# Performance work log

Measured on AMD Instinct MI355X. Metric: run time of the kernel, lower is better.

## Reference

```python
import jax, jax.numpy as jnp
from jax import lax
import numpy as np

ATTN = 32  # attn_size window
PAD, SOS = 1, 2


def setup_inputs() -> dict:
    key = jax.random.key(0)
    ks = jax.random.split(key, 20)
    B, L, V, E, H = 16, 64, 32000, 512, 512
    sc = 0.02
    inp = {
        "s_tensor": jax.random.randint(ks[0], (B, L), 0, V, dtype=jnp.int32),
        "parents_tensor": jax.random.randint(ks[1], (L,), 0, L, dtype=jnp.int32),
        "emb": jax.random.normal(ks[2], (V, E), jnp.float32) * sc,
        "W_hid": jax.random.normal(ks[3], (H, H), jnp.float32) * sc,
        "b_hid": jnp.zeros((H,), jnp.float32),
        "v_w": jax.random.normal(ks[4], (H,), jnp.float32) * sc,
        "v_b": jnp.zeros((1,), jnp.float32),
        "W_ctx": jax.random.normal(ks[5], (E + H, H), jnp.float32) * sc,
        "b_ctx": jnp.zeros((H,), jnp.float32),
        "W_ih": jax.random.normal(ks[6], (H, 4 * H), jnp.float32) * sc,
        "W_hh": jax.random.normal(ks[7], (H, 4 * H), jnp.float32) * sc,
        "b_lstm": jnp.zeros((4 * H,), jnp.float32),
        "W_glob": jax.random.normal(ks[8], (3 * H, V), jnp.float32) * sc,
        "b_glob": jnp.zeros((V,), jnp.float32),
        "w_sw": jax.random.normal(ks[9], (2 * H,), jnp.float32) * sc,
        "b_sw": jnp.zeros((1,), jnp.float32),
    }
    return inp


def _decode(emb, W_hid, b_hid, v_w, v_b, W_ctx, b_ctx, W_ih, W_hh, b_lstm,
            W_glob, b_glob, w_sw, b_sw, s_tensor, parents_tensor):
    B, L = s_tensor.shape
    H = W_hid.shape[0]
    A = ATTN
    # teacher forcing: input at step t is SOS for t=0, else s_tensor[:, t-1]
    inputs = jnp.concatenate(
        [jnp.full((B, 1), SOS, s_tensor.dtype), s_tensor[:, : L - 2]], axis=1)  # [B, L-1]
    targets = s_tensor[:, 1:]  # [B, L-1]
    hs_buf0 = jnp.zeros((B, A + L, H), jnp.float32)  # past decoder hidden states (A zero-pad prefix)
    h0 = jnp.zeros((B, H), jnp.float32)
    c0 = jnp.zeros((B, H), jnp.float32)

    def step(carry, xs):
        h, c, hs_buf = carry
        tok, tgt, par, t = xs
        x = emb[tok]  # [B, E]
        # memory = last A decoder hidden states (steps t-A .. t-1)
        mem = lax.dynamic_slice(hs_buf, (0, t, 0), (B, A, H))
        # Bahdanau-style scores: v^T tanh(W_hidden(h) + mem), masked to valid window
        q = h @ W_hid + b_hid  # [B, H]
        scores = jnp.tanh(q[:, None, :] + mem) @ v_w + v_b  # [B, A]
        valid = jnp.arange(A) >= (A - t)
        scores = jnp.where(valid[None, :], scores, -1e20)
        attn = jax.nn.softmax(scores, axis=1)
        context = jnp.einsum('ba,bah->bh', attn, mem)
        hid = jax.nn.selu(jnp.concatenate([x, context], axis=1) @ W_ctx + b_ctx)
        # single-step LSTM cell (PyTorch gate order i,f,g,o)
        gates = hid @ W_ih + h @ W_hh + b_lstm
        i, f, g, o = jnp.split(gates, 4, axis=1)
        c_new = jax.nn.sigmoid(f) * c + jax.nn.sigmoid(i) * jnp.tanh(g)
        h_new = jax.nn.sigmoid(o) * jnp.tanh(c_new)
        # parent hidden state
        p = jnp.clip(par, 0, jnp.maximum(t - 1, 0))
        h_par = lax.dynamic_slice(hs_buf, (0, A + p, 0), (B, 1, H))[:, 0]
        logits = jnp.concatenate([h_new, c_new, h_par], axis=1) @ W_glob + b_glob
        logp = jax.nn.log_softmax(logits, axis=1)
        s = jax.nn.sigmoid(jnp.concatenate([h_new, c_new], axis=1) @ w_sw + b_sw)  # [B,1]
        out = s[:, None] * logp if s.ndim == 1 else s * logp  # pointer switch on global dist
        nll = -jnp.take_along_axis(out, tgt[:, None].astype(jnp.int32), axis=1)[:, 0]
        nll = jnp.where(tgt != PAD, nll, 0.0)
        pred = jnp.argmax(out, axis=1).astype(jnp.int32)
        hs_buf = lax.dynamic_update_slice(hs_buf, h_new[:, None, :], (0, A + t, 0))
        return (h_new, c_new, hs_buf), (nll, pred)

    T = L - 1
    xs = (inputs.T, targets.T, parents_tensor[:T], jnp.arange(T, dtype=jnp.int32))
    _, (nlls, preds) = lax.scan(step, (h0, c0, hs_buf0), xs)
    loss = nlls.sum() / B
    return loss, preds.T  # [B, L-1] predicted tokens


def reference(s_tensor, parents_tensor, emb, W_hid, b_hid, v_w, v_b, W_ctx, b_ctx,
              W_ih, W_hh, b_lstm, W_glob, b_glob, w_sw, b_sw):
    return _decode(emb, W_hid, b_hid, v_w, v_b, W_ctx, b_ctx, W_ih, W_hh, b_lstm,
                   W_glob, b_glob, w_sw, b_sw, s_tensor, parents_tensor)
```

## Files before the change

kernel.cpp:

```cpp
#include <hip/hip_runtime.h>
#include <math.h>

#define BB 16
#define LL 64
#define TT 63
#define HH 512
#define AA 32
#define VV 32000
#define NCHUNK 250
#define CHW 128
#define TGRP 3
#define NTG 21
#define PAD_TOK 1
#define SOS_TOK 2
#define HSROW 96
#define ZK 1536
#define FLTMAX 3.402823466e38f

__device__ __forceinline__ float sigm(float x){ return 1.0f/(1.0f + __expf(-x)); }

__global__ __launch_bounds__(256) void k_pre(const int* __restrict__ s, const float* __restrict__ emb,
                      const float* __restrict__ Wctx, const float* __restrict__ bctx,
                      float* __restrict__ xwpre)
{
    int t = blockIdx.x >> 3;
    int jc = blockIdx.x & 7;
    int tid = threadIdx.x;
    int jj = tid & 63, bq = tid >> 6;
    int j = jc*64 + jj;
    __shared__ int toks[BB];
    __shared__ float xs[BB][HH];
    if (tid < BB) {
        int b = tid;
        toks[b] = (t == 0) ? SOS_TOK : s[b*LL + (t-1)];
    }
    __syncthreads();
    for (int i = tid; i < BB*HH; i += 256) {
        int b = i >> 9, k = i & 511;
        xs[b][k] = emb[(size_t)toks[b]*HH + k];
    }
    __syncthreads();
    float acc[4];
    #pragma unroll
    for (int u = 0; u < 4; u++) acc[u] = bctx[j];
    for (int k = 0; k < HH; k += 4) {
        float w0 = Wctx[(k+0)*HH+j], w1 = Wctx[(k+1)*HH+j],
              w2 = Wctx[(k+2)*HH+j], w3 = Wctx[(k+3)*HH+j];
        #pragma unroll
        for (int u = 0; u < 4; u++) {
            int b = bq*4 + u;
            float4 hv = *reinterpret_cast<const float4*>(&xs[b][k]);
            acc[u] = fmaf(hv.x, w0, acc[u]);
            acc[u] = fmaf(hv.y, w1, acc[u]);
            acc[u] = fmaf(hv.z, w2, acc[u]);
            acc[u] = fmaf(hv.w, w3, acc[u]);
        }
    }
    #pragma unroll
    for (int u = 0; u < 4; u++) {
        int b = bq*4 + u;
        xwpre[((size_t)t*BB + b)*HH + j] = acc[u];
    }
}

__global__ __launch_bounds__(256) void k_tw(const float* __restrict__ Wg, float4* __restrict__ Wt4b)
{
    int kg = blockIdx.x / 125;
    int cb = blockIdx.x % 125;
    int col = cb*256 + threadIdx.x;
    const float* w0 = Wg + (size_t)(4*kg)*VV + col;
    float4 v;
    v.x = w0[0];
    v.y = w0[VV];
    v.z = w0[2*VV];
    v.w = w0[3*VV];
    Wt4b[(size_t)(col >> 6)*(384*64) + kg*64 + (col & 63)] = v;
}

__global__ __launch_bounds__(256) void k_twl(const float* __restrict__ W, float4* __restrict__ WT)
{
    int kg = blockIdx.x >> 3;
    int cb = blockIdx.x & 7;
    int col = cb*256 + threadIdx.x;
    const float* w0 = W + (size_t)(4*kg)*2048 + col;
    float4 v;
    v.x = w0[0];
    v.y = w0[2048];
    v.z = w0[2*2048];
    v.w = w0[3*2048];
    WT[(size_t)kg*2048 + col] = v;
}

__device__ void finish_step(int tp, int b, int tid,
                            const int* __restrict__ s,
                            const float* __restrict__ lb,
                            const float* __restrict__ pmax,
                            const float* __restrict__ spart,
                            const float* __restrict__ bsw,
                            float* __restrict__ nll, float* __restrict__ out,
                            float* cv, int* ci, double* sdd, float* extra)
{
    float v = -FLTMAX;
    if (tid < NCHUNK) v = pmax[tid*BB + b];
    cv[tid] = v; __syncthreads();
    for (int sft = 256; sft >= 1; sft >>= 1) {
        if (tid < sft) cv[tid] = fmaxf(cv[tid], cv[tid+sft]);
        __syncthreads();
    }
    float gmax = cv[0];
    __syncthreads();

    const float* Lb = lb + (size_t)b*VV;
    double sd = 0.0;
    for (int col = tid; col < VV; col += 512) {
        float d1 = Lb[col] - gmax;
        double u = (double)d1, e;
        if (u < -0.25) {
            e = exp(u);
        } else {
            e = 1.0 + u*(1.0/7.0);
            e = 1.0 + u*e*(1.0/6.0);
            e = 1.0 + u*e*(1.0/5.0);
            e = 1.0 + u*e*(1.0/4.0);
            e = 1.0 + u*e*(1.0/3.0);
            e = 1.0 + u*e*(1.0/2.0);
            e = 1.0 + u*e;
        }
        sd += e;
    }
    sdd[tid] = sd; __syncthreads();
    for (int sft = 256; sft >= 1; sft >>= 1) {
        if (tid < sft) sdd[tid] += sdd[tid+sft];
        __syncthreads();
    }
    float logS = logf((float)sdd[0]);

    float z = bsw[0];
    #pragma unroll
    for (int i2 = 0; i2 < 8; i2++) z += spart[b*8 + i2];
    float sF = 1.0f/(1.0f + expf(-z));
    __syncthreads();

    int tg = s[b*LL + tp + 1];
    float best = -FLTMAX; int bidx = 0x7fffffff;
    for (int col = tid; col < VV; col += 512) {
        float d1 = Lb[col] - gmax;
        float d2 = d1 - logS;
        float pq = sF * d2;
        if (pq > best) { best = pq; bidx = col; }
        if (col == tg) extra[0] = pq;
    }
    cv[tid] = best; ci[tid] = bidx; __syncthreads();
    for (int sft = 256; sft >= 1; sft >>= 1) {
        if (tid < sft) {
            float v2 = cv[tid+sft]; int i2 = ci[tid+sft];
            if (v2 > cv[tid] || (v2 == cv[tid] && i2 < ci[tid])) { cv[tid] = v2; ci[tid] = i2; }
        }
        __syncthreads();
    }
    if (tid == 0) {
        out[1 + b*TT + tp] = (float)ci[0];
        nll[tp*BB + b] = (tg != PAD_TOK) ? -extra[0] : 0.f;
    }
    __syncthreads();
}

__global__ __launch_bounds__(512) void k_fin_all(
    int t0, const int* __restrict__ s,
    const float* __restrict__ lbBase, unsigned long long lbStride,
    const float* __restrict__ pmaxBase, unsigned long long pmaxStride,
    const float* __restrict__ spartAll, const float* __restrict__ bsw,
    float* __restrict__ nll, float* __restrict__ out)
{
    __shared__ float cv[512];
    __shared__ int   ci[512];
    __shared__ double sdd[512];
    __shared__ float extra[2];
    int idx = blockIdx.x >> 4;
    int tp = t0 + idx, b = blockIdx.x & 15;
    finish_step(tp, b, threadIdx.x, s,
                lbBase + (size_t)idx * lbStride,
                pmaxBase + (size_t)idx * pmaxStride,
                spartAll + (size_t)tp * 128,
                bsw, nll, out, cv, ci, sdd, extra);
}

__global__ __launch_bounds__(512) void k_attn(
    int t,
    const float* __restrict__ Whid, const float* __restrict__ bhid,
    const float* __restrict__ vw, const float* __restrict__ vb,
    const float* __restrict__ Wctx, const float* __restrict__ xwpre,
    const float* __restrict__ hs, float* __restrict__ hidg)
{
    int b = blockIdx.x, tid = threadIdx.x;
    __shared__ float hsh[HH], qs[HH], ctxs[HH];
    __shared__ float sc[AA], at[AA];
    const float* hp = hs + ((size_t)b*HSROW + (AA + t - 1))*HH;
    hsh[tid] = hp[tid];
    __syncthreads();
    {
        int j = tid;
        float acc = bhid[j];
        for (int k = 0; k < HH; k += 4) {
            float4 hv = *reinterpret_cast<const float4*>(&hsh[k]);
            acc = fmaf(hv.x, Whid[(k+0)*HH+j], acc);
            acc = fmaf(hv.y, Whid[(k+1)*HH+j], acc);
            acc = fmaf(hv.z, Whid[(k+2)*HH+j], acc);
            acc = fmaf(hv.w, Whid[(k+3)*HH+j], acc);
        }
        qs[j] = acc;
    }
    __syncthreads();
    {
        int w = tid >> 6, lane = tid & 63;
        for (int r = 0; r < 4; r++) {
            int a = w + 8*r;
            const float* mem = hs + ((size_t)b*HSROW + (t + a))*HH;
            float p = 0.f;
            for (int j = lane; j < HH; j += 64) p += tanhf(qs[j] + mem[j]) * vw[j];
            for (int m = 32; m >= 1; m >>= 1) p += __shfl_xor(p, m);
            if (lane == 0) sc[a] = (a >= AA - t) ? (p + vb[0]) : -1e20f;
        }
    }
    __syncthreads();
    if (tid < 64) {
        float v = (tid < 32) ? sc[tid] : -FLTMAX;
        float m = v;
        for (int sh = 16; sh >= 1; sh >>= 1) m = fmaxf(m, __shfl_xor(m, sh));
        float e = (tid < 32) ? __expf(v - m) : 0.f;
        float ss = e;
        for (int sh = 16; sh >= 1; sh >>= 1) ss += __shfl_xor(ss, sh);
        if (tid < 32) at[tid] = e / ss;
    }
    __syncthreads();
    {
        int j = tid;
        float ctx = 0.f;
        for (int a = 0; a < AA; a++)
            ctx += at[a] * hs[((size_t)b*HSROW + (t + a))*HH + j];
        ctxs[j] = ctx;
    }
    __syncthreads();
    {
        int j = tid;
        float acc = xwpre[((size_t)t*BB + b)*HH + j];
        const float* W2 = Wctx + (size_t)HH*HH;
        for (int k = 0; k < HH; k += 4) {
            float4 hv = *reinterpret_cast<const float4*>(&ctxs[k]);
            acc = fmaf(hv.x, W2[(k+0)*HH+j], acc);
            acc = fmaf(hv.y, W2[(k+1)*HH+j], acc);
            acc = fmaf(hv.z, W2[(k+2)*HH+j], acc);
            acc = fmaf(hv.w, W2[(k+3)*HH+j], acc);
        }
        const float scl = 1.0507009873554805f, al = 1.6732632423543772f;
        hidg[b*HH + j] = (acc > 0.f) ? scl*acc : scl*al*expm1f(acc);
    }
}

__global__ __launch_bounds__(256) void k_gates(
    int t, const int* __restrict__ parents,
    const float4* __restrict__ WihT, const float4* __restrict__ WhhT,
    const float* __restrict__ blstm, const float* __restrict__ wsw,
    const float* __restrict__ hidg, float* __restrict__ hs,
    float* __restrict__ cvec, float* __restrict__ spart,
    float* __restrict__ zbuf)
{
    int bid = blockIdx.x, b = bid >> 3, hc = bid & 7, h0 = hc*64;
    int tid = threadIdx.x, g = tid >> 6, jj = tid & 63, j = h0 + jj, col = g*HH + j;
    __shared__ float hid_s[HH], h_s[HH];
    __shared__ float gsl[4][64];
    const float* hp = hs + ((size_t)b*HSROW + (AA + t - 1))*HH;
    for (int k = tid; k < HH; k += 256) { hid_s[k] = hidg[b*HH + k]; h_s[k] = hp[k]; }
    __syncthreads();
    float acc = blstm[col];
    #pragma unroll 8
    for (int kg = 0; kg < 128; kg++) {
        float4 w = WihT[(size_t)kg*2048 + col];
        float4 hv = *reinterpret_cast<const float4*>(&hid_s[kg*4]);
        acc = fmaf(hv.x, w.x, acc);
        acc = fmaf(hv.y, w.y, acc);
        acc = fmaf(hv.z, w.z, acc);
        acc = fmaf(hv.w, w.w, acc);
    }
    #pragma unroll 8
    for (int kg = 0; kg < 128; kg++) {
        float4 w = WhhT[(size_t)kg*2048 + col];
        float4 hv = *reinterpret_cast<const float4*>(&h_s[kg*4]);
        acc = fmaf(hv.x, w.x, acc);
        acc = fmaf(hv.y, w.y, acc);
        acc = fmaf(hv.z, w.z, acc);
        acc = fmaf(hv.w, w.w, acc);
    }
    gsl[g][jj] = acc;
    __syncthreads();
    if (tid >= 64 && tid < 128) {
        int jj2 = tid - 64;
        int par = parents[t];
        int tm1 = (t - 1 > 0) ? (t - 1) : 0;
        int p = (par < 0) ? 0 : ((par > tm1) ? tm1 : par);
        float v = (t == 0) ? 0.f : hs[((size_t)b*HSROW + (AA + p))*HH + h0 + jj2];
        zbuf[(size_t)b*ZK + 2*HH + h0 + jj2] = v;
    }
    if (tid < 64) {
        float gi = gsl[0][jj], gf = gsl[1][jj], gg = gsl[2][jj], go = gsl[3][jj];
        float cp = cvec[b*HH + j];
        float cn = sigm(gf)*cp + sigm(gi)*tanhf(gg);
        float hn = sigm(go)*tanhf(cn);
        cvec[b*HH + j] = cn;
        hs[((size_t)b*HSROW + (AA + t))*HH + j] = hn;
        zbuf[(size_t)b*ZK + j] = hn;
        zbuf[(size_t)b*ZK + HH + j] = cn;
        float sp = hn*wsw[j] + cn*wsw[HH + j];
        for (int m = 32; m >= 1; m >>= 1) sp += __shfl_xor(sp, m);
        if (jj == 0) spart[b*8 + hc] = sp;
    }
}

template<int NT>
__device__ __forceinline__ void logits_body6(int chunk, int base_t,
    const float4* __restrict__ Wt4b, const float* __restrict__ bg,
    const float* __restrict__ zBase, size_t zStride,
    float* __restrict__ lbBase, size_t lbStride,
    float* __restrict__ pmaxBase, size_t pmaxStride,
    float* zs)
{
    int tid = threadIdx.x;
    int lane = tid & 63;
    int cg = lane & 31;
    int kh = lane >> 5;
    int b0 = (tid >> 6) * 4;
    const int BUF = NT*16*2*64;

    const float4* wt0 = Wt4b + (size_t)(chunk*2 + 0)*(384*64) + cg;
    const float4* wt1 = Wt4b + (size_t)(chunk*2 + 0)*(384*64) + cg + 32;
    const float4* wt2 = Wt4b + (size_t)(chunk*2 + 1)*(384*64) + cg;
    const float4* wt3 = Wt4b + (size_t)(chunk*2 + 1)*(384*64) + cg + 32;

    float acc[NT][4][4];
    #pragma unroll
    for (int tt = 0; tt < NT; tt++)
        #pragma unroll
        for (int cc = 0; cc < 4; cc++) {
            float binit = (kh == 0) ? bg[chunk*CHW + cg + 32*cc] : 0.f;
            #pragma unroll
            for (int u = 0; u < 4; u++) acc[tt][cc][u] = binit;
        }

    const int NF4 = NT*16*2*16;
    auto STAGE = [&](int sc, float* dst) {
        int kc = sc >> 2, sub = sc & 3;
        #pragma unroll
        for (int p = 0; p < NF4/256; p++) {
            int fi = tid + p*256;
            int kl4 = fi & 15, khs = (fi >> 4) & 1, uu = (fi >> 5) & 15, tt = fi >> 9;
            const float* src = zBase + (size_t)(base_t + tt)*zStride + kc*512
                             + (size_t)uu*ZK + khs*256 + sub*64 + kl4*4;
            *reinterpret_cast<float4*>(&dst[(((tt*16 + uu)*2 + khs)*64) + kl4*4]) =
                *reinterpret_cast<const float4*>(src);
        }
    };

    STAGE(0, zs);
    __syncthreads();
    for (int sc = 0; sc < 12; sc++) {
        float* cur = zs + (sc & 1)*BUF;
        if (sc + 1 < 12) STAGE(sc + 1, zs + ((sc + 1) & 1)*BUF);
        int kc = sc >> 2, sub = sc & 3;
        int kgb = kc*128 + kh*64 + sub*16;
        const float4* w0P = wt0 + (size_t)kgb*64;
        const float4* w1P = wt1 + (size_t)kgb*64;
        const float4* w2P = wt2 + (size_t)kgb*64;
        const float4* w3P = wt3 + (size_t)kgb*64;
        #pragma unroll 4
        for (int kl = 0; kl < 16; kl++) {
            float4 w0 = w0P[kl*64];
            float4 w1 = w1P[kl*64];
            float4 w2 = w2P[kl*64];
            float4 w3 = w3P[kl*64];
            #pragma unroll
            for (int tt = 0; tt < NT; tt++) {
                #pragma unroll
                for (int u = 0; u < 4; u++) {
                    float4 z = *reinterpret_cast<const float4*>(
                        &cur[(((tt*16 + (b0 + u))*2 + kh)*64) + kl*4]);
                    acc[tt][0][u] = fmaf(z.x, w0.x, fmaf(z.y, w0.y, fmaf(z.z, w0.z, fmaf(z.w, w0.w, acc[tt][0][u]))));
                    acc[tt][1][u] = fmaf(z.x, w1.x, fmaf(z.y, w1.y, fmaf(z.z, w1.z, fmaf(z.w, w1.w, acc[tt][1][u]))));
                    acc[tt][2][u] = fmaf(z.x, w2.x, fmaf(z.y, w2.y, fmaf(z.z, w2.z, fmaf(z.w, w2.w, acc[tt][2][u]))));
                    acc[tt][3][u] = fmaf(z.x, w3.x, fmaf(z.y, w3.y, fmaf(z.z, w3.z, fmaf(z.w, w3.w, acc[tt][3][u]))));
                }
            }
        }
        __syncthreads();
    }

    #pragma unroll
    for (int tt = 0; tt < NT; tt++) {
        float* lb   = lbBase   + (size_t)(base_t + tt)*lbStride;
        float* pmax = pmaxBase + (size_t)(base_t + tt)*pmaxStride;
        #pragma unroll
        for (int u = 0; u < 4; u++) {
            float vmax = -FLTMAX;
            #pragma unroll
            for (int cc = 0; cc < 4; cc++) {
                float a = acc[tt][cc][u];
                float oth = __shfl_xor(a, 32);
                float tot = a + oth;
                if (kh == 0) lb[(size_t)(b0 + u)*VV + chunk*CHW + cg + 32*cc] = tot;
                vmax = fmaxf(vmax, tot);
            }
            for (int m = 16; m >= 1; m >>= 1) vmax = fmaxf(vmax, __shfl_xor(vmax, m));
            if (lane == 0) pmax[chunk*BB + b0 + u] = vmax;
        }
    }
}

__global__ __launch_bounds__(256) void k_logits_mega3(
    const float4* __restrict__ Wt4b, const float* __restrict__ bg,
    const float* __restrict__ zBase,
    float* __restrict__ lbBase, float* __restrict__ pmaxBase)
{
    __shared__ float zs[2*TGRP*16*2*64];
    logits_body6<TGRP>(blockIdx.y, blockIdx.x * TGRP, Wt4b, bg,
                       zBase, (size_t)BB*ZK, lbBase, 512000, pmaxBase, 4000, zs);
}

__global__ __launch_bounds__(256) void k_logits_T1(
    const float4* __restrict__ Wt4b, const float* __restrict__ bg,
    const float* __restrict__ zbuf,
    float* __restrict__ lb, float* __restrict__ pmax)
{
    __shared__ float zs[2*1*16*2*64];
    logits_body6<1>(blockIdx.x, 0, Wt4b, bg, zbuf, 0, lb, 0, pmax, 0, zs);
}

__global__ __launch_bounds__(256) void k_logits_F(
    const float* __restrict__ Wg, const float* __restrict__ bg,
    const float* __restrict__ zbuf,
    float* __restrict__ lb, float* __restrict__ pmax)
{
    int tid = threadIdx.x;
    int chunk = blockIdx.x;
    int lane = tid & 63;
    int cg = lane & 31;
    int kh = lane >> 5;
    int b0 = (tid >> 6) * 4;

    float acc[4][4];
    #pragma unroll
    for (int cc = 0; cc < 4; cc++) {
        float binit = (kh == 0) ? bg[chunk*CHW + cg + 32*cc] : 0.f;
        #pragma unroll
        for (int u = 0; u < 4; u++) acc[cc][u] = binit;
    }

    for (int kc = 0; kc < 3; kc++) {
        const float* zb = zbuf + kc*512 + (size_t)b0*ZK;
        #pragma unroll 2
        for (int k4 = 0; k4 < 64; k4++) {
            int kb = kh*256 + k4*4;
            const float* wr = Wg + (size_t)(kc*512 + kb)*VV + chunk*CHW + cg;
            float4 w[4];
            #pragma unroll
            for (int cc = 0; cc < 4; cc++) {
                w[cc].x = wr[32*cc];
                w[cc].y = wr[(size_t)VV + 32*cc];
                w[cc].z = wr[(size_t)2*VV + 32*cc];
                w[cc].w = wr[(size_t)3*VV + 32*cc];
            }
            #pragma unroll
            for (int u = 0; u < 4; u++) {
                float4 z = *reinterpret_cast<const float4*>(&zb[(size_t)u*ZK + kb]);
                #pragma unroll
                for (int cc = 0; cc < 4; cc++)
                    acc[cc][u] = fmaf(z.x, w[cc].x, fmaf(z.y, w[cc].y, fmaf(z.z, w[cc].z, fmaf(z.w, w[cc].w, acc[cc][u]))));
            }
        }
    }

    #pragma unroll
    for (int u = 0; u < 4; u++) {
        float vmax = -FLTMAX;
        #pragma unroll
        for (int cc = 0; cc < 4; cc++) {
            float a = acc[cc][u];
            float oth = __shfl_xor(a, 32);
            float tot = a + oth;
            if (kh == 0) lb[(size_t)(b0 + u)*VV + chunk*CHW + cg + 32*cc] = tot;
            vmax = fmaxf(vmax, tot);
        }
        for (int m = 16; m >= 1; m >>= 1) vmax = fmaxf(vmax, __shfl_xor(vmax, m));
        if (lane == 0) pmax[chunk*BB + b0 + u] = vmax;
    }
}

__global__ __launch_bounds__(256) void k_final_loss(
    const float* __restrict__ nll, float* __restrict__ out)
{
    __shared__ double cs2[256];
    int tid = threadIdx.x;
    double psm = 0.0;
    for (int i = tid; i < TT*BB; i += 256) psm += (double)nll[i];
    cs2[tid] = psm; __syncthreads();
    for (int sft = 128; sft >= 1; sft >>= 1) {
        if (tid < sft) cs2[tid] += cs2[tid+sft];
        __syncthreads();
    }
    if (tid == 0) out[0] = (float)(cs2[0] / (double)BB);
}

extern "C" void kernel_launch(void* const* d_in, const int* in_sizes, int n_in,
                              void* d_out, int out_size, void* d_ws, size_t ws_size,
                              hipStream_t stream)
{
    const int*   s_tok = (const int*)  d_in[0];
    const int*   par   = (const int*)  d_in[1];
    const float* emb   = (const float*)d_in[2];
    const float* Whid  = (const float*)d_in[3];
    const float* bhid  = (const float*)d_in[4];
    const float* vw    = (const float*)d_in[5];
    const float* vb    = (const float*)d_in[6];
    const float* Wctx  = (const float*)d_in[7];
    const float* bctx  = (const float*)d_in[8];
    const float* Wih   = (const float*)d_in[9];
    const float* Whh   = (const float*)d_in[10];
    const float* blstm = (const float*)d_in[11];
    const float* Wg    = (const float*)d_in[12];
    const float* bg    = (const float*)d_in[13];
    const float* wsw   = (const float*)d_in[14];
    const float* bsw   = (const float*)d_in[15];
    float* out = (float*)d_out;

    size_t ws_f = ws_size / sizeof(float);
    const size_t base_f = 786432 + 8192 + 516096 + 8192;
    const size_t com_f  = 8064 + 1008 + 2*1048576;
    const size_t full_f = base_f + com_f + (size_t)63*4000 + (size_t)63*512000
                        + (size_t)63*24576 + 49152000;
    const size_t mid_f  = base_f + com_f + 4000 + 512000 + 24576 + 49152000;
    int mode = (ws_f >= full_f) ? 2 : ((ws_f >= mid_f) ? 1 : 0);

    float* ws = (float*)d_ws;
    size_t off = 0;
    float* hs      = ws + off; off += 786432;
    float* cvec    = ws + off; off += 8192;
    float* xwpre   = ws + off; off += 516096;
    float* hidg    = ws + off; off += 8192;
    float* pmaxAll = ws + off; off += (mode == 2) ? (size_t)63*4000 : 4000;
    float* spartAll= ws + off; off += 8064;
    float* nll     = ws + off; off += 1008;
    float* zbufAll = ws + off; off += (mode == 2) ? (size_t)63*24576 : 24576;
    float* lbAll   = ws + off; off += (mode == 2) ? (size_t)63*512000 : 512000;
    float4* WihT   = (float4*)(ws + off); off += 1048576;
    float4* WhhT   = (float4*)(ws + off); off += 1048576;
    float4* Wt4b   = (float4*)(ws + off);

    hipMemsetAsync(hs, 0, (786432 + 8192) * sizeof(float), stream);

    hipLaunchKernelGGL(k_twl, dim3(1024), dim3(256), 0, stream, Wih, WihT);
    hipLaunchKernelGGL(k_twl, dim3(1024), dim3(256), 0, stream, Whh, WhhT);
    if (mode >= 1) {
        hipLaunchKernelGGL(k_tw, dim3(384*125), dim3(256), 0, stream, Wg, Wt4b);
    }
    hipLaunchKernelGGL(k_pre, dim3(TT*8), dim3(256), 0, stream, s_tok, emb, Wctx, bctx, xwpre);

    if (mode == 2) {
        for (int t = 0; t < TT; t++) {
            hipLaunchKernelGGL(k_attn, dim3(BB), dim3(512), 0, stream,
                t, Whid, bhid, vw, vb, Wctx, xwpre, hs, hidg);
            hipLaunchKernelGGL(k_gates, dim3(128), dim3(256), 0, stream,
                t, par, WihT, WhhT, blstm, wsw, hidg, hs, cvec,
                spartAll + (size_t)t*128, zbufAll + (size_t)t*BB*ZK);
        }
        hipLaunchKernelGGL(k_logits_mega3, dim3(NTG, NCHUNK), dim3(256), 0, stream,
            Wt4b, bg, zbufAll, lbAll, pmaxAll);
        hipLaunchKernelGGL(k_fin_all, dim3(TT*BB), dim3(512), 0, stream,
            0, s_tok, lbAll, (unsigned long long)512000,
            pmaxAll, (unsigned long long)4000,
            spartAll, bsw, nll, out);
    } else {
        for (int t = 0; t < TT; t++) {
            hipLaunchKernelGGL(k_attn, dim3(BB), dim3(512), 0, stream,
                t, Whid, bhid, vw, vb, Wctx, xwpre, hs, hidg);
            hipLaunchKernelGGL(k_gates, dim3(128), dim3(256), 0, stream,
                t, par, WihT, WhhT, blstm, wsw, hidg, hs, cvec,
                spartAll + (size_t)t*128, zbufAll);
            if (mode >= 1) {
                hipLaunchKernelGGL(k_logits_T1, dim3(NCHUNK), dim3(256), 0, stream,
                    Wt4b, bg, zbufAll, lbAll, pmaxAll);
            } else {
                hipLaunchKernelGGL(k_logits_F, dim3(NCHUNK), dim3(256), 0, stream,
                    Wg, bg, zbufAll, lbAll, pmaxAll);
            }
            hipLaunchKernelGGL(k_fin_all, dim3(BB), dim3(512), 0, stream,
                t, s_tok, lbAll, (unsigned long long)0, pmaxAll, (unsigned long long)0,
                spartAll, bsw, nll, out);
        }
    }
    hipLaunchKernelGGL(k_final_loss, dim3(1), dim3(256), 0, stream, nll, out);
}
```

Before: 4.767 ms.

## Fuse recurrent attention and LSTM steps into one cooperative persistent kernel

Replaces the 126 per-step launches of the attention and gate kernels with one cooperative kernel of 128 blocks that loops over timesteps and uses grid-wide syncs between the attention and gate phases. The attention work is rewritten for 256-thread blocks so it runs inside the persistent grid, on the first 16 blocks. The goal is to remove kernel launch overhead and inter-kernel gaps on the serial recurrence. The trade-off is that attention uses half as many threads per batch row, and each step now pays for two grid barriers. If cooperative launch is unavailable or fails, the old per-step launch loop is used.

After: 13.27 ms. +178.3%, slower.

```diff
diff --git a/kernel.cpp b/kernel.cpp
--- a/kernel.cpp
+++ b/kernel.cpp
@@ -1,5 +1,8 @@
 #include <hip/hip_runtime.h>
+#include <hip/hip_cooperative_groups.h>
 #include <math.h>
+
+namespace cg = cooperative_groups;
 
 #define BB 16
 #define LL 64
@@ -185,21 +188,21 @@
                 bsw, nll, out, cv, ci, sdd, extra);
 }
 
-__global__ __launch_bounds__(512) void k_attn(
-    int t,
+__device__ __forceinline__ void attn256(int t, int ab, int tid,
     const float* __restrict__ Whid, const float* __restrict__ bhid,
     const float* __restrict__ vw, const float* __restrict__ vb,
-    const float* __restrict__ Wctx, const float* __restrict__ xwpre,
-    const float* __restrict__ hs, float* __restrict__ hidg)
-{
-    int b = blockIdx.x, tid = threadIdx.x;
-    __shared__ float hsh[HH], qs[HH], ctxs[HH];
-    __shared__ float sc[AA], at[AA];
-    const float* hp = hs + ((size_t)b*HSROW + (AA + t - 1))*HH;
+    const float* __restrict__ W2, const float* __restrict__ xwpre,
+    const float* __restrict__ hs, float* __restrict__ hidg,
+    float* hsh, float* qs, float* ctxs, float* sc, float* at)
+{
+    const float* hp = hs + ((size_t)ab*HSROW + (AA + t - 1))*HH;
     hsh[tid] = hp[tid];
-    __syncthreads();
-    {
-        int j = tid;
+    hsh[tid + 256] = hp[tid + 256];
+    __syncthreads();
+
+    #pragma unroll
+    for (int jo = 0; jo < HH; jo += 256) {
+        int j = tid + jo;
         float acc = bhid[j];
         for (int k = 0; k < HH; k += 4) {
             float4 hv = *reinterpret_cast<const float4*>(&hsh[k]);
@@ -211,11 +214,12 @@
         qs[j] = acc;
     }
     __syncthreads();
+
     {
         int w = tid >> 6, lane = tid & 63;
-        for (int r = 0; r < 4; r++) {
-            int a = w + 8*r;
-            const float* mem = hs + ((size_t)b*HSROW + (t + a))*HH;
+        for (int r = 0; r < 8; r++) {
+            int a = w + 4*r;
+            const float* mem = hs + ((size_t)ab*HSROW + (t + a))*HH;
             float p = 0.f;
             for (int j = lane; j < HH; j += 64) p += tanhf(qs[j] + mem[j]) * vw[j];
             for (int m = 32; m >= 1; m >>= 1) p += __shfl_xor(p, m);
@@ -223,6 +227,7 @@
         }
     }
     __syncthreads();
+
     if (tid < 64) {
         float v = (tid < 32) ? sc[tid] : -FLTMAX;
         float m = v;
@@ -233,18 +238,21 @@
         if (tid < 32) at[tid] = e / ss;
     }
     __syncthreads();
-    {
-        int j = tid;
+
+    #pragma unroll
+    for (int jo = 0; jo < HH; jo += 256) {
+        int j = tid + jo;
         float ctx = 0.f;
         for (int a = 0; a < AA; a++)
-            ctx += at[a] * hs[((size_t)b*HSROW + (t + a))*HH + j];
+            ctx += at[a] * hs[((size_t)ab*HSROW + (t + a))*HH + j];
         ctxs[j] = ctx;
     }
     __syncthreads();
-    {
-        int j = tid;
-        float acc = xwpre[((size_t)t*BB + b)*HH + j];
-        const float* W2 = Wctx + (size_t)HH*HH;
+
+    #pragma unroll
+    for (int jo = 0; jo < HH; jo += 256) {
+        int j = tid + jo;
+        float acc = xwpre[((size_t)t*BB + ab)*HH + j];
         for (int k = 0; k < HH; k += 4) {
             float4 hv = *reinterpret_cast<const float4*>(&ctxs[k]);
             acc = fmaf(hv.x, W2[(k+0)*HH+j], acc);
@@ -253,25 +261,20 @@
             acc = fmaf(hv.w, W2[(k+3)*HH+j], acc);
         }
         const float scl = 1.0507009873554805f, al = 1.6732632423543772f;
-        hidg[b*HH + j] = (acc > 0.f) ? scl*acc : scl*al*expm1f(acc);
-    }
-}
-
-__global__ __launch_bounds__(256) void k_gates(
-    int t, const int* __restrict__ parents,
+        hidg[ab*HH + j] = (acc > 0.f) ? scl*acc : scl*al*expm1f(acc);
+    }
+}
+
+__device__ __forceinline__ void gates256(int t, int b, int hc, int tid,
+    const int* __restrict__ parents,
     const float4* __restrict__ WihT, const float4* __restrict__ WhhT,
     const float* __restrict__ blstm, const float* __restrict__ wsw,
-    const float* __restrict__ hidg, float* __restrict__ hs,
-    float* __restrict__ cvec, float* __restrict__ spart,
-    float* __restrict__ zbuf)
-{
-    int bid = blockIdx.x, b = bid >> 3, hc = bid & 7, h0 = hc*64;
-    int tid = threadIdx.x, g = tid >> 6, jj = tid & 63, j = h0 + jj, col = g*HH + j;
-    __shared__ float hid_s[HH], h_s[HH];
-    __shared__ float gsl[4][64];
-    const float* hp = hs + ((size_t)b*HSROW + (AA + t - 1))*HH;
-    for (int k = tid; k < HH; k += 256) { hid_s[k] = hidg[b*HH + k]; h_s[k] = hp[k]; }
-    __syncthreads();
+    float* __restrict__ hs, float* __restrict__ cvec,
+    float* __restrict__ spart, float* __restrict__ zbuf,
+    float* hid_s, float* h_s, float (*gsl)[64])
+{
+    int h0 = hc*64;
+    int g = tid >> 6, jj = tid & 63, j = h0 + jj, col = g*HH + j;
     float acc = blstm[col];
     #pragma unroll 8
     for (int kg = 0; kg < 128; kg++) {
@@ -316,6 +319,133 @@
     }
 }
 
+__global__ __launch_bounds__(256) void k_persist(
+    const int* __restrict__ parents,
+    const float* __restrict__ Whid, const float* __restrict__ bhid,
+    const float* __restrict__ vw, const float* __restrict__ vb,
+    const float* __restrict__ Wctx, const float* __restrict__ xwpre,
+    const float4* __restrict__ WihT, const float4* __restrict__ WhhT,
+    const float* __restrict__ blstm, const float* __restrict__ wsw,
+    float* __restrict__ hs, float* __restrict__ cvec,
+    float* __restrict__ spartAll, float* __restrict__ zbufAll,
+    float* __restrict__ hidg)
+{
+    cg::grid_group grid = cg::this_grid();
+    int bid = blockIdx.x, tid = threadIdx.x;
+    int b = bid >> 3, hc = bid & 7;
+    __shared__ float hsh[HH], qs[HH], ctxs[HH], hid_s[HH];
+    __shared__ float sc[AA], at[AA];
+    __shared__ float gsl[4][64];
+    const float* W2 = Wctx + (size_t)HH*HH;
+
+    for (int t = 0; t < TT; t++) {
+        if (bid < BB) {
+            attn256(t, bid, tid, Whid, bhid, vw, vb, W2, xwpre, hs, hidg,
+                    hsh, qs, ctxs, sc, at);
+        }
+        grid.sync();
+
+        const float* hp = hs + ((size_t)b*HSROW + (AA + t - 1))*HH;
+        for (int k = tid; k < HH; k += 256) { hid_s[k] = hidg[b*HH + k]; hsh[k] = hp[k]; }
+        __syncthreads();
+        gates256(t, b, hc, tid, parents, WihT, WhhT, blstm, wsw,
+                 hs, cvec, spartAll + (size_t)t*128, zbufAll + (size_t)t*BB*ZK,
+                 hid_s, hsh, gsl);
+        grid.sync();
+    }
+}
+
+__global__ __launch_bounds__(512) void k_attn(
+    int t,
+    const float* __restrict__ Whid, const float* __restrict__ bhid,
+    const float* __restrict__ vw, const float* __restrict__ vb,
+    const float* __restrict__ Wctx, const float* __restrict__ xwpre,
+    const float* __restrict__ hs, float* __restrict__ hidg)
+{
+    int b = blockIdx.x, tid = threadIdx.x;
+    __shared__ float hsh[HH], qs[HH], ctxs[HH];
+    __shared__ float sc[AA], at[AA];
+    const float* hp = hs + ((size_t)b*HSROW + (AA + t - 1))*HH;
+    hsh[tid] = hp[tid];
+    __syncthreads();
+    {
+        int j = tid;
+        float acc = bhid[j];
+        for (int k = 0; k < HH; k += 4) {
+            float4 hv = *reinterpret_cast<const float4*>(&hsh[k]);
+            acc = fmaf(hv.x, Whid[(k+0)*HH+j], acc);
+            acc = fmaf(hv.y, Whid[(k+1)*HH+j], acc);
+            acc = fmaf(hv.z, Whid[(k+2)*HH+j], acc);
+            acc = fmaf(hv.w, Whid[(k+3)*HH+j], acc);
+        }
+        qs[j] = acc;
+    }
+    __syncthreads();
+    {
+        int w = tid >> 6, lane = tid & 63;
+        for (int r = 0; r < 4; r++) {
+            int a = w + 8*r;
+            const float* mem = hs + ((size_t)b*HSROW + (t + a))*HH;
+            float p = 0.f;
+            for (int j = lane; j < HH; j += 64) p += tanhf(qs[j] + mem[j]) * vw[j];
+            for (int m = 32; m >= 1; m >>= 1) p += __shfl_xor(p, m);
+            if (lane == 0) sc[a] = (a >= AA - t) ? (p + vb[0]) : -1e20f;
+        }
+    }
+    __syncthreads();
+    if (tid < 64) {
+        float v = (tid < 32) ? sc[tid] : -FLTMAX;
+        float m = v;
+        for (int sh = 16; sh >= 1; sh >>= 1) m = fmaxf(m, __shfl_xor(m, sh));
+        float e = (tid < 32) ? __expf(v - m) : 0.f;
+        float ss = e;
+        for (int sh = 16; sh >= 1; sh >>= 1) ss += __shfl_xor(ss, sh);
+        if (tid < 32) at[tid] = e / ss;
+    }
+    __syncthreads();
+    {
+        int j = tid;
+        float ctx = 0.f;
+        for (int a = 0; a < AA; a++)
+            ctx += at[a] * hs[((size_t)b*HSROW + (t + a))*HH + j];
+        ctxs[j] = ctx;
+    }
+    __syncthreads();
+    {
+        int j = tid;
+        float acc = xwpre[((size_t)t*BB + b)*HH + j];
+        const float* W2 = Wctx + (size_t)HH*HH;
+        for (int k = 0; k < HH; k += 4) {
+            float4 hv = *reinterpret_cast<const float4*>(&ctxs[k]);
+            acc = fmaf(hv.x, W2[(k+0)*HH+j], acc);
+            acc = fmaf(hv.y, W2[(k+1)*HH+j], acc);
+            acc = fmaf(hv.z, W2[(k+2)*HH+j], acc);
+            acc = fmaf(hv.w, W2[(k+3)*HH+j], acc);
+        }
+        const float scl = 1.0507009873554805f, al = 1.6732632423543772f;
+        hidg[b*HH + j] = (acc > 0.f) ? scl*acc : scl*al*expm1f(acc);
+    }
+}
+
+__global__ __launch_bounds__(256) void k_gates(
+    int t, const int* __restrict__ parents,
+    const float4* __restrict__ WihT, const float4* __restrict__ WhhT,
+    const float* __restrict__ blstm, const float* __restrict__ wsw,
+    const float* __restrict__ hidg, float* __restrict__ hs,
+    float* __restrict__ cvec, float* __restrict__ spart,
+    float* __restrict__ zbuf)
+{
+    int bid = blockIdx.x, b = bid >> 3, hc = bid & 7;
+    int tid = threadIdx.x;
+    __shared__ float hid_s[HH], h_s[HH];
+    __shared__ float gsl[4][64];
+    const float* hp = hs + ((size_t)b*HSROW + (AA + t - 1))*HH;
+    for (int k = tid; k < HH; k += 256) { hid_s[k] = hidg[b*HH + k]; h_s[k] = hp[k]; }
+    __syncthreads();
+    gates256(t, b, hc, tid, parents, WihT, WhhT, blstm, wsw,
+             hs, cvec, spart, zbuf, hid_s, h_s, gsl);
+}
+
 template<int NT>
 __device__ __forceinline__ void logits_body6(int chunk, int base_t,
     const float4* __restrict__ Wt4b, const float* __restrict__ bg,
@@ -326,29 +456,29 @@
 {
     int tid = threadIdx.x;
     int lane = tid & 63;
-    int cg = lane & 31;
+    int cg2 = lane & 31;
     int kh = lane >> 5;
     int b0 = (tid >> 6) * 4;
     const int BUF = NT*16*2*64;
 
-    const float4* wt0 = Wt4b + (size_t)(chunk*2 + 0)*(384*64) + cg;
-    const float4* wt1 = Wt4b + (size_t)(chunk*2 + 0)*(384*64) + cg + 32;
-    const float4* wt2 = Wt4b + (size_t)(chunk*2 + 1)*(384*64) + cg;
-    const float4* wt3 = Wt4b + (size_t)(chunk*2 + 1)*(384*64) + cg + 32;
+    const float4* wt0 = Wt4b + (size_t)(chunk*2 + 0)*(384*64) + cg2;
+    const float4* wt1 = Wt4b + (size_t)(chunk*2 + 0)*(384*64) + cg2 + 32;
+    const float4* wt2 = Wt4b + (size_t)(chunk*2 + 1)*(384*64) + cg2;
+    const float4* wt3 = Wt4b + (size_t)(chunk*2 + 1)*(384*64) + cg2 + 32;
 
     float acc[NT][4][4];
     #pragma unroll
     for (int tt = 0; tt < NT; tt++)
         #pragma unroll
         for (int cc = 0; cc < 4; cc++) {
-            float binit = (kh == 0) ? bg[chunk*CHW + cg + 32*cc] : 0.f;
+            float binit = (kh == 0) ? bg[chunk*CHW + cg2 + 32*cc] : 0.f;
             #pragma unroll
             for (int u = 0; u < 4; u++) acc[tt][cc][u] = binit;
         }
 
     const int NF4 = NT*16*2*16;
-    auto STAGE = [&](int sc, float* dst) {
-        int kc = sc >> 2, sub = sc & 3;
+    auto STAGE = [&](int sc2, float* dst) {
+        int kc = sc2 >> 2, sub = sc2 & 3;
         #pragma unroll
         for (int p = 0; p < NF4/256; p++) {
             int fi = tid + p*256;
@@ -362,10 +492,10 @@
 
     STAGE(0, zs);
     __syncthreads();
-    for (int sc = 0; sc < 12; sc++) {
-        float* cur = zs + (sc & 1)*BUF;
-        if (sc + 1 < 12) STAGE(sc + 1, zs + ((sc + 1) & 1)*BUF);
-        int kc = sc >> 2, sub = sc & 3;
+    for (int sc2 = 0; sc2 < 12; sc2++) {
+        float* cur = zs + (sc2 & 1)*BUF;
+        if (sc2 + 1 < 12) STAGE(sc2 + 1, zs + ((sc2 + 1) & 1)*BUF);
+        int kc = sc2 >> 2, sub = sc2 & 3;
         int kgb = kc*128 + kh*64 + sub*16;
         const float4* w0P = wt0 + (size_t)kgb*64;
         const float4* w1P = wt1 + (size_t)kgb*64;
@@ -405,7 +535,7 @@
                 float a = acc[tt][cc][u];
                 float oth = __shfl_xor(a, 32);
                 float tot = a + oth;
-                if (kh == 0) lb[(size_t)(b0 + u)*VV + chunk*CHW + cg + 32*cc] = tot;
+                if (kh == 0) lb[(size_t)(b0 + u)*VV + chunk*CHW + cg2 + 32*cc] = tot;
                 vmax = fmaxf(vmax, tot);
             }
             for (int m = 16; m >= 1; m >>= 1) vmax = fmaxf(vmax, __shfl_xor(vmax, m));
@@ -441,14 +571,14 @@
     int tid = threadIdx.x;
     int chunk = blockIdx.x;
     int lane = tid & 63;
-    int cg = lane & 31;
+    int cg2 = lane & 31;
     int kh = lane >> 5;
     int b0 = (tid >> 6) * 4;
 
     float acc[4][4];
     #pragma unroll
     for (int cc = 0; cc < 4; cc++) {
-        float binit = (kh == 0) ? bg[chunk*CHW + cg + 32*cc] : 0.f;
+        float binit = (kh == 0) ? bg[chunk*CHW + cg2 + 32*cc] : 0.f;
         #pragma unroll
         for (int u = 0; u < 4; u++) acc[cc][u] = binit;
     }
@@ -458,7 +588,7 @@
         #pragma unroll 2
         for (int k4 = 0; k4 < 64; k4++) {
             int kb = kh*256 + k4*4;
-            const float* wr = Wg + (size_t)(kc*512 + kb)*VV + chunk*CHW + cg;
+            const float* wr = Wg + (size_t)(kc*512 + kb)*VV + chunk*CHW + cg2;
             float4 w[4];
             #pragma unroll
             for (int cc = 0; cc < 4; cc++) {
@@ -485,7 +615,7 @@
             float a = acc[cc][u];
             float oth = __shfl_xor(a, 32);
             float tot = a + oth;
-            if (kh == 0) lb[(size_t)(b0 + u)*VV + chunk*CHW + cg + 32*cc] = tot;
+            if (kh == 0) lb[(size_t)(b0 + u)*VV + chunk*CHW + cg2 + 32*cc] = tot;
             vmax = fmaxf(vmax, tot);
         }
         for (int m = 16; m >= 1; m >>= 1) vmax = fmaxf(vmax, __shfl_xor(vmax, m));
@@ -563,12 +693,26 @@
     hipLaunchKernelGGL(k_pre, dim3(TT*8), dim3(256), 0, stream, s_tok, emb, Wctx, bctx, xwpre);
 
     if (mode == 2) {
-        for (int t = 0; t < TT; t++) {
-            hipLaunchKernelGGL(k_attn, dim3(BB), dim3(512), 0, stream,
-                t, Whid, bhid, vw, vb, Wctx, xwpre, hs, hidg);
-            hipLaunchKernelGGL(k_gates, dim3(128), dim3(256), 0, stream,
-                t, par, WihT, WhhT, blstm, wsw, hidg, hs, cvec,
-                spartAll + (size_t)t*128, zbufAll + (size_t)t*BB*ZK);
+        int coop = 0;
+        hipDeviceGetAttribute(&coop, hipDeviceAttributeCooperativeLaunch, 0);
+        hipError_t ce = hipErrorUnknown;
+        if (coop) {
+            void* args[] = {
+                (void*)&par, (void*)&Whid, (void*)&bhid, (void*)&vw, (void*)&vb,
+                (void*)&Wctx, (void*)&xwpre, (void*)&WihT, (void*)&WhhT,
+                (void*)&blstm, (void*)&wsw, (void*)&hs, (void*)&cvec,
+                (void*)&spartAll, (void*)&zbufAll, (void*)&hidg };
+            ce = hipLaunchCooperativeKernel((const void*)k_persist,
+                                            dim3(128), dim3(256), args, 0, stream);
+        }
+        if (ce != hipSuccess) {
+            for (int t = 0; t < TT; t++) {
+                hipLaunchKernelGGL(k_attn, dim3(BB), dim3(512), 0, stream,
+                    t, Whid, bhid, vw, vb, Wctx, xwpre, hs, hidg);
+                hipLaunchKernelGGL(k_gates, dim3(128), dim3(256), 0, stream,
+                    t, par, WihT, WhhT, blstm, wsw, hidg, hs, cvec,
+                    spartAll + (size_t)t*128, zbufAll + (size_t)t*BB*ZK);
+            }
         }
         hipLaunchKernelGGL(k_logits_mega3, dim3(NTG, NCHUNK), dim3(256), 0, stream,
             Wt4b, bg, zbufAll, lbAll, pmaxAll);
```
